# Kernel tuning notes

Hardware: AMD Instinct MI355X
Metric: run time of the kernel (lower is better)

Reference implementation:

```python
import jax, jax.numpy as jnp
import numpy as np

B, S, D, H, L = 8, 1024, 768, 12, 12
HD = D // H          # head dim 64
F = 4 * D            # mlp hidden 3072
N_SEG = 8            # ~images packed per sequence


def layer_norm(x, w, b, eps=1e-5):
    m = jnp.mean(x, axis=-1, keepdims=True)
    v = jnp.mean((x - m) ** 2, axis=-1, keepdims=True)
    return (x - m) / jnp.sqrt(v + eps) * w + b


def setup_inputs() -> dict:
    key = jax.random.key(0)
    ks = jax.random.split(key, 16)
    packed_tokens = jax.random.normal(ks[0], (B, S, D), dtype=jnp.float32)
    # block-diagonal mask from sorted segment ids (True = disallowed, torch bool-mask convention)
    seg = jnp.sort(jax.random.randint(ks[1], (S,), 0, N_SEG))
    attn_mask = seg[:, None] != seg[None, :]
    std = 0.02
    p = {
        'packed_tokens': packed_tokens,
        'attn_mask': attn_mask,
        'ln1_w': jnp.ones((L, D), jnp.float32),
        'ln1_b': jnp.zeros((L, D), jnp.float32),
        'wqkv': jax.random.normal(ks[2], (L, D, 3 * D), jnp.float32) * std,
        'bqkv': jnp.zeros((L, 3 * D), jnp.float32),
        'wo': jax.random.normal(ks[3], (L, D, D), jnp.float32) * std,
        'bo': jnp.zeros((L, D), jnp.float32),
        'ln2_w': jnp.ones((L, D), jnp.float32),
        'ln2_b': jnp.zeros((L, D), jnp.float32),
        'w1': jax.random.normal(ks[4], (L, D, F), jnp.float32) * std,
        'b1': jnp.zeros((L, F), jnp.float32),
        'w2': jax.random.normal(ks[5], (L, F, D), jnp.float32) * std,
        'b2': jnp.zeros((L, D), jnp.float32),
        'norm_w': jnp.ones((D,), jnp.float32),
        'norm_b': jnp.zeros((D,), jnp.float32),
    }
    return p


def attention(x, mask, wqkv, bqkv, wo, bo):
    qkv = x @ wqkv + bqkv                                  # [B,S,3D]
    q, k, v = jnp.split(qkv, 3, axis=-1)
    q = q.reshape(B, S, H, HD)
    k = k.reshape(B, S, H, HD)
    v = v.reshape(B, S, H, HD)
    scores = jnp.einsum('bqhd,bkhd->bhqk', q, k) / jnp.sqrt(jnp.asarray(HD, x.dtype))
    neg = jnp.asarray(jnp.finfo(scores.dtype).min, scores.dtype)
    scores = jnp.where(mask[None, None], neg, scores)
    probs = jax.nn.softmax(scores, axis=-1)
    out = jnp.einsum('bhqk,bkhd->bqhd', probs, v).reshape(B, S, D)
    return out @ wo + bo


def reference(packed_tokens, attn_mask, ln1_w, ln1_b, wqkv, bqkv, wo, bo,
              ln2_w, ln2_b, w1, b1, w2, b2, norm_w, norm_b):
    x = packed_tokens  # dropout = identity in eval
    for l in range(L):
        n = layer_norm(x, ln1_w[l], ln1_b[l])
        x = x + attention(n, attn_mask, wqkv[l], bqkv[l], wo[l], bo[l])
        n = layer_norm(x, ln2_w[l], ln2_b[l])
        h = jax.nn.gelu(n @ w1[l] + b1[l], approximate=False)
        x = x + h @ w2[l] + b2[l]
    return layer_norm(x, norm_w, norm_b)
```

## Files before the change

### kernel.cpp

```cpp
#include <hip/hip_runtime.h>
#include <hip/hip_bf16.h>
#include <math.h>

typedef __hip_bfloat16 bf16_t;
typedef _Float16 h16;
typedef _Float16 f16x8 __attribute__((ext_vector_type(8)));
typedef float f32x4 __attribute__((ext_vector_type(4)));

constexpr int B = 8;
constexpr int S = 1024;
constexpr int D = 768;
constexpr int H = 12;
constexpr int HD = 64;
constexpr int F = 3072;
constexpr int L = 12;
constexpr int T = B * S;


typedef const __attribute__((address_space(1))) void g_void;
typedef __attribute__((address_space(3))) void s_void;
#define GLD16(gp, lp) __builtin_amdgcn_global_load_lds((g_void*)(gp), (s_void*)(lp), 16, 0, 0)

__device__ __forceinline__ float ldf(const void* p, size_t i, int f32) {
    return f32 ? ((const float*)p)[i] : __bfloat162float(((const bf16_t*)p)[i]);
}

__global__ void dtype_sniff_kernel(const uint32_t* __restrict__ w, int* __restrict__ meta) {
    if (threadIdx.x == 0) meta[1] = (w[0] == 0x3F800000u) ? 1 : 0;
}

__global__ __launch_bounds__(256) void mask_sniff_kernel(const uint32_t* __restrict__ mask,
                                                         int* __restrict__ meta) {
    __shared__ int firstw;
    if (threadIdx.x == 0) firstw = 1 << 30;
    __syncthreads();
    int idx = threadIdx.x;
    uint32_t v0 = mask[idx];
    uint32_t v1 = mask[256 + idx];
    uint32_t v2 = mask[512 + idx];
    uint32_t v3 = mask[768 + idx];
    int best = 1 << 30;
    if (v3) best = 768 + idx;
    if (v2) best = 512 + idx;
    if (v1) best = 256 + idx;
    if (v0) best = idx;
    atomicMin(&firstw, best);
    __syncthreads();
    if (threadIdx.x == 0) {
        int fi = firstw;
        meta[0] = (fi < (1 << 30) && mask[fi] == 1u) ? 1 : 0;
    }
}

__global__ __launch_bounds__(256) void rowrange_kernel(const void* __restrict__ mask,
                                                       int* __restrict__ meta) {
    int q = blockIdx.x;
    int f = meta[0];
    int lo = S, hi = -1;
    for (int j = threadIdx.x; j < S; j += 256) {
        int v = f ? ((const int*)mask)[(size_t)q * S + j]
                  : (int)((const unsigned char*)mask)[(size_t)q * S + j];
        if (v == 0) { lo = min(lo, j); hi = max(hi, j); }
    }
    for (int off = 32; off > 0; off >>= 1) {
        lo = min(lo, __shfl_xor(lo, off));
        hi = max(hi, __shfl_xor(hi, off));
    }
    __shared__ int slo[4], shi[4];
    int wv = threadIdx.x >> 6;
    if ((threadIdx.x & 63) == 0) { slo[wv] = lo; shi[wv] = hi; }
    __syncthreads();
    if (threadIdx.x == 0) {
        lo = min(min(slo[0], slo[1]), min(slo[2], slo[3]));
        hi = max(max(shi[0], shi[1]), max(shi[2], shi[3]));
        if (lo > hi) { lo = q; hi = q; }
        meta[16 + q] = lo;
        meta[16 + S + q] = hi;
    }
}

__global__ __launch_bounds__(256) void cast_kernel(const void* __restrict__ in,
                                                   const int* __restrict__ meta,
                                                   float* __restrict__ out, int n) {
    int f32 = meta[1];
    int i = blockIdx.x * 256 + threadIdx.x;
    if (i < n) out[i] = ldf(in, i, f32);
}

template <bool EXTERNAL>
__global__ __launch_bounds__(256) void ln_kernel(const float* __restrict__ x,
                                                 const void* __restrict__ w, size_t wo_,
                                                 const void* __restrict__ b, size_t bo_,
                                                 const int* __restrict__ meta,
                                                 void* __restrict__ out) {
    int f32 = meta[1];
    int t = blockIdx.x;
    int tid = threadIdx.x;
    __shared__ float xs[D];
    __shared__ float red[16];
    const float* xp = x + (size_t)t * D;

    float s = 0.f;
#pragma unroll
    for (int i = 0; i < 3; i++) {
        float v = xp[tid + i * 256];
        xs[tid + i * 256] = v;
        s += v;
    }
    for (int off = 32; off > 0; off >>= 1) s += __shfl_xor(s, off);
    int wv = tid >> 6, lane = tid & 63;
    if (lane == 0) red[wv] = s;
    __syncthreads();
    float mean = (red[0] + red[1] + red[2] + red[3]) * (1.0f / 768.0f);

    float s2 = 0.f;
#pragma unroll
    for (int i = 0; i < 3; i++) {
        float d = xs[tid + i * 256] - mean;
        s2 += d * d;
    }
    for (int off = 32; off > 0; off >>= 1) s2 += __shfl_xor(s2, off);
    if (lane == 0) red[8 + wv] = s2;
    __syncthreads();
    float var = (red[8] + red[9] + red[10] + red[11]) * (1.0f / 768.0f);
    float rstd = rsqrtf(var + 1e-5f);

#pragma unroll
    for (int i = 0; i < 3; i++) {
        int d = tid + i * 256;
        float v = (xs[d] - mean) * rstd * ldf(w, wo_ + d, f32) + ldf(b, bo_ + d, f32);
        size_t idx = (size_t)t * D + d;
        if (EXTERNAL) {
            if (f32) ((float*)out)[idx] = v;
            else ((bf16_t*)out)[idx] = __float2bfloat16(v);
        } else {
            ((h16*)out)[idx] = (h16)v;
        }
    }
}

__global__ __launch_bounds__(256) void wtrans_kernel(const void* __restrict__ W, size_t woff,
                                                     const int* __restrict__ meta,
                                                     h16* __restrict__ wt,
                                                     int K, int N) {
    int f32 = meta[1];
    __shared__ float tile[32][33];
    int n0 = blockIdx.x * 32, k0 = blockIdx.y * 32;
    int tx = threadIdx.x & 31, ty = threadIdx.x >> 5;
#pragma unroll
    for (int i = 0; i < 4; i++) {
        int k = ty + i * 8;
        tile[k][tx] = ldf(W, woff + (size_t)(k0 + k) * N + n0 + tx, f32);
    }
    __syncthreads();
#pragma unroll
    for (int i = 0; i < 4; i++) {
        int nn = ty + i * 8;
        wt[(size_t)(n0 + nn) * K + k0 + tx] = (h16)tile[tx][nn];
    }
}

template <bool GELU, bool ADD>
__global__ __launch_bounds__(256) void mgemm_kernel(const h16* __restrict__ A,
                                                    const h16* __restrict__ Bt,
                                                    const void* __restrict__ bias, size_t boff,
                                                    const int* __restrict__ meta,
                                                    void* __restrict__ C,
                                                    int M, int N, int K) {
    int f32 = meta[1];
    __shared__ h16 Als[128 * 32];
    __shared__ h16 Bls[128 * 32];
    int tid = threadIdx.x;
    int lane = tid & 63;
    int wv = tid >> 6;
    int wy = wv >> 1, wx = wv & 1;
    int m0 = blockIdx.y * 128, n0 = blockIdx.x * 128;

    int row0 = tid >> 2, kc0 = (tid & 3) * 8;
    int row1 = 64 + row0;
    const h16* ag0 = A + (size_t)(m0 + row0) * K + kc0;
    const h16* ag1 = A + (size_t)(m0 + row1) * K + kc0;
    const h16* bg0 = Bt + (size_t)(n0 + row0) * K + kc0;
    const h16* bg1 = Bt + (size_t)(n0 + row1) * K + kc0;
    h16* la0 = Als + (size_t)tid * 8;
    h16* la1 = Als + (size_t)(256 + tid) * 8;
    h16* lb0 = Bls + (size_t)tid * 8;
    h16* lb1 = Bls + (size_t)(256 + tid) * 8;

    const h16* pa = Als + ((wy * 64) + (lane & 15)) * 32 + (lane >> 4) * 8;
    const h16* pb = Bls + ((wx * 64) + (lane & 15)) * 32 + (lane >> 4) * 8;

    f32x4 acc[4][4];
#pragma unroll
    for (int i = 0; i < 4; i++)
#pragma unroll
        for (int j = 0; j < 4; j++) acc[i][j] = (f32x4){0.f, 0.f, 0.f, 0.f};

    for (int k0 = 0; k0 < K; k0 += 32) {
        GLD16(ag0, la0); GLD16(ag1, la1);
        GLD16(bg0, lb0); GLD16(bg1, lb1);
        ag0 += 32; ag1 += 32; bg0 += 32; bg1 += 32;
        __syncthreads();

        f16x8 af[4], bf[4];
#pragma unroll
        for (int i = 0; i < 4; i++) af[i] = *(const f16x8*)(pa + i * 16 * 32);
#pragma unroll
        for (int j = 0; j < 4; j++) bf[j] = *(const f16x8*)(pb + j * 16 * 32);
#pragma unroll
        for (int i = 0; i < 4; i++)
#pragma unroll
            for (int j = 0; j < 4; j++)
                acc[i][j] = __builtin_amdgcn_mfma_f32_16x16x32_f16(af[i], bf[j], acc[i][j], 0, 0, 0);
        __syncthreads();
    }

    int col_base = n0 + wx * 64 + (lane & 15);
    int row_base = m0 + wy * 64 + (lane >> 4) * 4;
#pragma unroll
    for (int j = 0; j < 4; j++) {
        int nn = col_base + j * 16;
        float bv = ldf(bias, boff + nn, f32);
#pragma unroll
        for (int i = 0; i < 4; i++) {
#pragma unroll
            for (int r = 0; r < 4; r++) {
                int mm = row_base + i * 16 + r;
                float v = acc[i][j][r] + bv;
                if (GELU) v = 0.5f * v * (1.0f + erff(v * 0.70710678118654752f));
                size_t idx = (size_t)mm * N + nn;
                if (ADD) ((float*)C)[idx] += v;
                else ((h16*)C)[idx] = (h16)v;
            }
        }
    }
}

template <bool GELU, bool ADD>
__global__ __launch_bounds__(256) void gemm_kernel(const h16* __restrict__ A,
                                                   const void* __restrict__ W, size_t wo_,
                                                   const void* __restrict__ bias, size_t bo_,
                                                   const int* __restrict__ meta,
                                                   void* __restrict__ C,
                                                   int M, int N, int K) {
    int f32 = meta[1];
    __shared__ float As[16][65];
    __shared__ float Bs[16][65];
    int tid = threadIdx.y * 16 + threadIdx.x;
    int m0 = blockIdx.y * 64, n0 = blockIdx.x * 64;
    float c[4][4] = {};

    for (int k0 = 0; k0 < K; k0 += 16) {
#pragma unroll
        for (int i = 0; i < 4; i++) {
            int flat = tid + i * 256;
            int m = flat >> 4, k = flat & 15;
            As[k][m] = (float)A[(size_t)(m0 + m) * K + k0 + k];
        }
#pragma unroll
        for (int i = 0; i < 4; i++) {
            int flat = tid + i * 256;
            int k = flat >> 6, n = flat & 63;
            Bs[k][n] = ldf(W, wo_ + (size_t)(k0 + k) * N + n0 + n, f32);
        }
        __syncthreads();
#pragma unroll
        for (int kk = 0; kk < 16; kk++) {
            float a[4], bb[4];
#pragma unroll
            for (int i = 0; i < 4; i++) a[i] = As[kk][threadIdx.y * 4 + i];
#pragma unroll
            for (int j = 0; j < 4; j++) bb[j] = Bs[kk][threadIdx.x * 4 + j];
#pragma unroll
            for (int i = 0; i < 4; i++)
#pragma unroll
                for (int j = 0; j < 4; j++) c[i][j] += a[i] * bb[j];
        }
        __syncthreads();
    }

#pragma unroll
    for (int i = 0; i < 4; i++) {
        int m = m0 + threadIdx.y * 4 + i;
#pragma unroll
        for (int j = 0; j < 4; j++) {
            int n = n0 + threadIdx.x * 4 + j;
            float v = c[i][j] + ldf(bias, bo_ + n, f32);
            if (GELU) v = 0.5f * v * (1.0f + erff(v * 0.70710678118654752f));
            size_t idx = (size_t)m * N + n;
            if (ADD) ((float*)C)[idx] += v;
            else ((h16*)C)[idx] = (h16)v;
        }
    }
}

__global__ __launch_bounds__(256) void mattn_kernel(const h16* __restrict__ qkv,
                                                    const int* __restrict__ meta,
                                                    h16* __restrict__ ao) {
    const int* rowlo = meta + 16;
    const int* rowhi = meta + 16 + S;
    int bh = blockIdx.y;
    int b = bh / H, h = bh % H;
    int q0 = blockIdx.x * 64;
    int tid = threadIdx.x;
    int lane = tid & 63;
    int w = tid >> 6;
    int qw = q0 + w * 16;

    __shared__ h16 Vt[64 * 64];
    __shared__ h16 Ps[4][16 * 64];

    const size_t rs = 3 * D;
    const h16* base = qkv + (size_t)b * S * rs;

    int rl = rowlo[q0 + lane], rh = rowhi[q0 + lane];
    for (int off = 32; off > 0; off >>= 1) {
        rl = min(rl, __shfl_xor(rl, off));
        rh = max(rh, __shfl_xor(rh, off));
    }
    int c_lo = rl & ~63;
    int c_hi = rh + 1;

    int qrow = qw + (lane >> 4) * 4;
    int mlo[4], mhi[4];
#pragma unroll
    for (int r = 0; r < 4; r++) { mlo[r] = rowlo[qrow + r]; mhi[r] = rowhi[qrow + r]; }

    f16x8 qf[2];
    {
        const h16* qp = base + (size_t)(qw + (lane & 15)) * rs + h * 64 + (lane >> 4) * 8;
        qf[0] = *(const f16x8*)(qp);
        qf[1] = *(const f16x8*)(qp + 32);
    }

    float m_r[4], l_r[4];
    f32x4 o[4];
#pragma unroll
    for (int r = 0; r < 4; r++) { m_r[r] = -1e30f; l_r[r] = 0.f; }
#pragma unroll
    for (int jf = 0; jf < 4; jf++) o[jf] = (f32x4){0.f, 0.f, 0.f, 0.f};

    for (int c0 = c_lo; c0 < c_hi; c0 += 64) {
        {
            int k = tid & 63, d0 = (tid >> 6) * 16;
            const h16* vp = base + (size_t)(c0 + k) * rs + 2 * D + h * 64 + d0;
            f16x8 v0 = *(const f16x8*)vp;
            f16x8 v1 = *(const f16x8*)(vp + 8);
#pragma unroll
            for (int j = 0; j < 8; j++) {
                int d = d0 + j;
                Vt[(d * 64 + k) ^ ((d & 7) << 3)] = v0[j];
                d = d0 + 8 + j;
                Vt[(d * 64 + k) ^ ((d & 7) << 3)] = v1[j];
            }
        }

        f32x4 s[4];
#pragma unroll
        for (int jf = 0; jf < 4; jf++) {
            const h16* kp = base + (size_t)(c0 + jf * 16 + (lane & 15)) * rs + D + h * 64 + (lane >> 4) * 8;
            f16x8 kf0 = *(const f16x8*)kp;
            f16x8 kf1 = *(const f16x8*)(kp + 32);
            s[jf] = (f32x4){0.f, 0.f, 0.f, 0.f};
            s[jf] = __builtin_amdgcn_mfma_f32_16x16x32_f16(qf[0], kf0, s[jf], 0, 0, 0);
            s[jf] = __builtin_amdgcn_mfma_f32_16x16x32_f16(qf[1], kf1, s[jf], 0, 0, 0);
        }

        float pmax[4];
#pragma unroll
        for (int r = 0; r < 4; r++) pmax[r] = -3.0e38f;
#pragma unroll
        for (int jf = 0; jf < 4; jf++) {
            int k = c0 + jf * 16 + (lane & 15);
#pragma unroll
            for (int r = 0; r < 4; r++) {
                float v = (k < mlo[r] || k > mhi[r]) ? -3.0e38f : s[jf][r] * 0.125f;
                s[jf][r] = v;
                pmax[r] = fmaxf(pmax[r], v);
            }
        }
#pragma unroll
        for (int off = 1; off < 16; off <<= 1)
#pragma unroll
            for (int r = 0; r < 4; r++) pmax[r] = fmaxf(pmax[r], __shfl_xor(pmax[r], off));

        float scl[4];
#pragma unroll
        for (int r = 0; r < 4; r++) {
            float mn = fmaxf(m_r[r], pmax[r]);
            scl[r] = __expf(m_r[r] - mn);
            m_r[r] = mn;
            l_r[r] *= scl[r];
        }
#pragma unroll
        for (int jf = 0; jf < 4; jf++) {
#pragma unroll
            for (int r = 0; r < 4; r++) {
                float e = __expf(s[jf][r] - m_r[r]);
                l_r[r] += e;
                int q = (lane >> 4) * 4 + r;
                int k = jf * 16 + (lane & 15);
                Ps[w][(q * 64 + k) ^ ((q & 7) << 3)] = (h16)e;
            }
        }
#pragma unroll
        for (int jf = 0; jf < 4; jf++)
#pragma unroll
            for (int r = 0; r < 4; r++) o[jf][r] *= scl[r];

        __syncthreads();

        f16x8 pa0, pa1;
        {
            int q = lane & 15;
            int e0 = q * 64 + (lane >> 4) * 8;
            int e1 = q * 64 + 32 + (lane >> 4) * 8;
            pa0 = *(const f16x8*)&Ps[w][e0 ^ ((q & 7) << 3)];
            pa1 = *(const f16x8*)&Ps[w][e1 ^ ((q & 7) << 3)];
        }
#pragma unroll
        for (int jf = 0; jf < 4; jf++) {
            int d = jf * 16 + (lane & 15);
            int e0 = d * 64 + (lane >> 4) * 8;
            int e1 = d * 64 + 32 + (lane >> 4) * 8;
            f16x8 vb0 = *(const f16x8*)&Vt[e0 ^ ((d & 7) << 3)];
            f16x8 vb1 = *(const f16x8*)&Vt[e1 ^ ((d & 7) << 3)];
            o[jf] = __builtin_amdgcn_mfma_f32_16x16x32_f16(pa0, vb0, o[jf], 0, 0, 0);
            o[jf] = __builtin_amdgcn_mfma_f32_16x16x32_f16(pa1, vb1, o[jf], 0, 0, 0);
        }
        __syncthreads();
    }

#pragma unroll
    for (int off = 1; off < 16; off <<= 1)
#pragma unroll
        for (int r = 0; r < 4; r++) l_r[r] += __shfl_xor(l_r[r], off);
#pragma unroll
    for (int jf = 0; jf < 4; jf++) {
        int d = jf * 16 + (lane & 15);
#pragma unroll
        for (int r = 0; r < 4; r++) {
            float inv = (l_r[r] > 0.f) ? 1.0f / l_r[r] : 0.f;
            int q = qw + (lane >> 4) * 4 + r;
            ao[(size_t)(b * S + q) * D + h * 64 + d] = (h16)(o[jf][r] * inv);
        }
    }
}

__global__ __launch_bounds__(512) void attn_kernel(const h16* __restrict__ qkv,
                                                   const int* __restrict__ meta,
                                                   h16* __restrict__ ao) {
    const int* rowlo = meta + 16;
    const int* rowhi = meta + 16 + S;
    int bh = blockIdx.x;
    int b = bh / H, h = bh % H;
    int q0 = blockIdx.y * 8;
    int tid = threadIdx.x;
    int qr = tid >> 6;
    int lane = tid & 63;
    int q = q0 + qr;

    __shared__ float qs[8][64];
    __shared__ float sc[8][S];
    __shared__ float kv[64][65];

    const size_t rowstride = 3 * D;
    const h16* qkv_b = qkv + (size_t)b * S * rowstride;

    qs[qr][lane] = (float)qkv_b[(size_t)(q0 + qr) * rowstride + h * 64 + lane];

    int lo = rowlo[q], hi = rowhi[q];
    int blo = S, bhi = -1;
#pragma unroll
    for (int i = 0; i < 8; i++) {
        blo = min(blo, rowlo[q0 + i]);
        bhi = max(bhi, rowhi[q0 + i]);
    }
    int c_lo = (blo / 64) * 64;
    int c_hi = bhi + 1;
    int c_up = c_lo + ((c_hi - c_lo + 63) / 64) * 64;

    for (int c0 = c_lo; c0 < c_hi; c0 += 64) {
        __syncthreads();
#pragma unroll
        for (int i = 0; i < 8; i++) {
            int flat = tid + i * 512;
            int jj = flat >> 6, dd = flat & 63;
            kv[jj][dd] = (float)qkv_b[(size_t)(c0 + jj) * rowstride + D + h * 64 + dd];
        }
        __syncthreads();
        float acc = 0.f;
#pragma unroll
        for (int d = 0; d < 64; d++) acc += qs[qr][d] * kv[lane][d];
        int j = c0 + lane;
        bool msk = (j < lo) || (j > hi);
        sc[qr][j] = msk ? -3.0e38f : acc * 0.125f;
    }
    __syncthreads();

    float m = -3.4e38f;
    for (int j = c_lo + lane; j < c_up; j += 64) m = fmaxf(m, sc[qr][j]);
    for (int off = 32; off > 0; off >>= 1) m = fmaxf(m, __shfl_xor(m, off));
    float sum = 0.f;
    for (int j = c_lo + lane; j < c_up; j += 64) {
        float e = expf(sc[qr][j] - m);
        sc[qr][j] = e;
        sum += e;
    }
    for (int off = 32; off > 0; off >>= 1) sum += __shfl_xor(sum, off);
    float inv = (sum > 0.f) ? 1.0f / sum : 0.f;

    float out = 0.f;
    for (int c0 = c_lo; c0 < c_hi; c0 += 64) {
        __syncthreads();
#pragma unroll
        for (int i = 0; i < 8; i++) {
            int flat = tid + i * 512;
            int jj = flat >> 6, dd = flat & 63;
            kv[jj][dd] = (float)qkv_b[(size_t)(c0 + jj) * rowstride + 2 * D + h * 64 + dd];
        }
        __syncthreads();
#pragma unroll
        for (int jj = 0; jj < 64; jj++) out += sc[qr][c0 + jj] * kv[jj][lane];
    }
    out *= inv;
    ao[((size_t)(b * S + q)) * D + h * 64 + lane] = (h16)out;
}

__global__ __launch_bounds__(256) void sentinel_kernel(uint32_t* __restrict__ out, int nwords) {
    int i = blockIdx.x * 256 + threadIdx.x;
    if (i < nwords) out[i] = 0x3F803F80u;
}

extern "C" void kernel_launch(void* const* d_in, const int* in_sizes, int n_in,
                              void* d_out, int out_size, void* d_ws, size_t ws_size,
                              hipStream_t stream) {
    const void* packed = d_in[0];
    const void* mask   = d_in[1];
    const void* ln1w   = d_in[2];
    const void* ln1b   = d_in[3];
    const void* wqkv   = d_in[4];
    const void* bqkv   = d_in[5];
    const void* wo     = d_in[6];
    const void* bo     = d_in[7];
    const void* ln2w   = d_in[8];
    const void* ln2b   = d_in[9];
    const void* w1     = d_in[10];
    const void* b1     = d_in[11];
    const void* w2     = d_in[12];
    const void* b2     = d_in[13];
    const void* normw  = d_in[14];
    const void* normb  = d_in[15];

    size_t x_b   = (size_t)T * D * 4;
    size_t n_b   = (size_t)T * D * 2;
    size_t big_b = (size_t)T * F * 2;
    size_t need_old = 16384 + x_b + n_b + big_b;
    size_t wt_elems = (size_t)3 * D * D + (size_t)D * D + (size_t)D * F + (size_t)F * D;
    size_t need_new = need_old + wt_elems * 2 ;

    if (ws_size < need_old) {
        int nwords = out_size / 2;
        sentinel_kernel<<<(nwords + 255) / 256, 256, 0, stream>>>((uint32_t*)d_out, nwords);
        return;
    }

    int* meta = (int*)d_ws;
    float* x  = (float*)((char*)d_ws + 16384);
    h16* n    = (h16*)((char*)x + x_b);
    h16* big  = (h16*)((char*)n + n_b);

    dtype_sniff_kernel<<<1, 64, 0, stream>>>((const uint32_t*)ln1w, meta);
    mask_sniff_kernel<<<1, 256, 0, stream>>>((const uint32_t*)mask, meta);
    rowrange_kernel<<<S, 256, 0, stream>>>(mask, meta);
    cast_kernel<<<(T * D + 255) / 256, 256, 0, stream>>>(packed, meta, x, T * D);

    if (ws_size >= need_new) {
        h16* wts = (h16*)((char*)big + big_b);
        h16* qkvT = wts;
        h16* woT  = qkvT + (size_t)3 * D * D;
        h16* w1T  = woT + (size_t)D * D;
        h16* w2T  = w1T + (size_t)D * F;

        for (int l = 0; l < L; l++) {
            wtrans_kernel<<<dim3(3 * D / 32, D / 32), 256, 0, stream>>>(
                wqkv, (size_t)l * D * 3 * D, meta, qkvT, D, 3 * D);
            wtrans_kernel<<<dim3(D / 32, D / 32), 256, 0, stream>>>(
                wo, (size_t)l * D * D, meta, woT, D, D);
            wtrans_kernel<<<dim3(F / 32, D / 32), 256, 0, stream>>>(
                w1, (size_t)l * D * F, meta, w1T, D, F);
            wtrans_kernel<<<dim3(D / 32, F / 32), 256, 0, stream>>>(
                w2, (size_t)l * F * D, meta, w2T, F, D);

            ln_kernel<false><<<T, 256, 0, stream>>>(x, ln1w, (size_t)l * D, ln1b, (size_t)l * D, meta, n);
            mgemm_kernel<false, false><<<dim3(3 * D / 128, T / 128), 256, 0, stream>>>(
                n, qkvT, bqkv, (size_t)l * 3 * D, meta, big, T, 3 * D, D);
            mattn_kernel<<<dim3(S / 64, B * H), 256, 0, stream>>>(big, meta, n);
            mgemm_kernel<false, true><<<dim3(D / 128, T / 128), 256, 0, stream>>>(
                n, woT, bo, (size_t)l * D, meta, x, T, D, D);
            ln_kernel<false><<<T, 256, 0, stream>>>(x, ln2w, (size_t)l * D, ln2b, (size_t)l * D, meta, n);
            mgemm_kernel<true, false><<<dim3(F / 128, T / 128), 256, 0, stream>>>(
                n, w1T, b1, (size_t)l * F, meta, big, T, F, D);
            mgemm_kernel<false, true><<<dim3(D / 128, T / 128), 256, 0, stream>>>(
                big, w2T, b2, (size_t)l * D, meta, x, T, D, F);
        }
    } else {
        dim3 thr(16, 16);
        for (int l = 0; l < L; l++) {
            ln_kernel<false><<<T, 256, 0, stream>>>(x, ln1w, (size_t)l * D, ln1b, (size_t)l * D, meta, n);
            gemm_kernel<false, false><<<dim3(3 * D / 64, T / 64), thr, 0, stream>>>(
                n, wqkv, (size_t)l * D * 3 * D, bqkv, (size_t)l * 3 * D, meta, big, T, 3 * D, D);
            attn_kernel<<<dim3(B * H, S / 8), 512, 0, stream>>>(big, meta, n);
            gemm_kernel<false, true><<<dim3(D / 64, T / 64), thr, 0, stream>>>(
                n, wo, (size_t)l * D * D, bo, (size_t)l * D, meta, x, T, D, D);
            ln_kernel<false><<<T, 256, 0, stream>>>(x, ln2w, (size_t)l * D, ln2b, (size_t)l * D, meta, n);
            gemm_kernel<true, false><<<dim3(F / 64, T / 64), thr, 0, stream>>>(
                n, w1, (size_t)l * D * F, b1, (size_t)l * F, meta, big, T, F, D);
            gemm_kernel<false, true><<<dim3(D / 64, T / 64), thr, 0, stream>>>(
                big, w2, (size_t)l * F * D, b2, (size_t)l * D, meta, x, T, D, F);
        }
    }
    ln_kernel<true><<<T, 256, 0, stream>>>(x, normw, 0, normb, 0, meta, d_out);
}
```

Measured before the change: 4.473 ms.

## Double-buffer MFMA GEMM LDS, swizzle layout, and split-K residual GEMMs with atomics

Adds a two-stage LDS double buffer so global-to-LDS loads of the next K tile overlap MFMA work on the current one, dropping one barrier per iteration. Applies an XOR swizzle to the LDS K offsets to cut bank conflicts on the fragment reads. Splits K for the output projection (2-way) and the second MLP GEMM (4-way) across blockIdx.z, accumulating into the fp32 residual with atomicAdd, so these 6x64-tile GEMMs get more blocks. Atomics add contention and make the summation order nondeterministic.

```diff
diff --git a/kernel.cpp b/kernel.cpp
--- a/kernel.cpp
+++ b/kernel.cpp
@@ -166,29 +166,29 @@
                                                     const void* __restrict__ bias, size_t boff,
                                                     const int* __restrict__ meta,
                                                     void* __restrict__ C,
-                                                    int M, int N, int K) {
+                                                    int M, int N, int K, int Kc) {
     int f32 = meta[1];
-    __shared__ h16 Als[128 * 32];
-    __shared__ h16 Bls[128 * 32];
+    __shared__ h16 Als[2][128 * 32];
+    __shared__ h16 Bls[2][128 * 32];
     int tid = threadIdx.x;
     int lane = tid & 63;
     int wv = tid >> 6;
     int wy = wv >> 1, wx = wv & 1;
     int m0 = blockIdx.y * 128, n0 = blockIdx.x * 128;
-
-    int row0 = tid >> 2, kc0 = (tid & 3) * 8;
+    int kz = blockIdx.z * Kc;
+
+    int row0 = tid >> 2;
     int row1 = 64 + row0;
-    const h16* ag0 = A + (size_t)(m0 + row0) * K + kc0;
-    const h16* ag1 = A + (size_t)(m0 + row1) * K + kc0;
-    const h16* bg0 = Bt + (size_t)(n0 + row0) * K + kc0;
-    const h16* bg1 = Bt + (size_t)(n0 + row1) * K + kc0;
-    h16* la0 = Als + (size_t)tid * 8;
-    h16* la1 = Als + (size_t)(256 + tid) * 8;
-    h16* lb0 = Bls + (size_t)tid * 8;
-    h16* lb1 = Bls + (size_t)(256 + tid) * 8;
-
-    const h16* pa = Als + ((wy * 64) + (lane & 15)) * 32 + (lane >> 4) * 8;
-    const h16* pb = Bls + ((wx * 64) + (lane & 15)) * 32 + (lane >> 4) * 8;
+    int kbs = (((tid & 3) * 16) ^ ((row0 & 3) << 4)) >> 1;
+    const h16* ag0 = A + (size_t)(m0 + row0) * K + kz + kbs;
+    const h16* ag1 = A + (size_t)(m0 + row1) * K + kz + kbs;
+    const h16* bg0 = Bt + (size_t)(n0 + row0) * K + kz + kbs;
+    const h16* bg1 = Bt + (size_t)(n0 + row1) * K + kz + kbs;
+
+    int arow = (lane & 15);
+    int akb = ((((lane >> 4) * 16) ^ ((arow & 3) << 4)) >> 1);
+    int aoff = (wy * 64 + arow) * 32 + akb;
+    int boff2 = (wx * 64 + arow) * 32 + akb;
 
     f32x4 acc[4][4];
 #pragma unroll
@@ -196,12 +196,25 @@
 #pragma unroll
         for (int j = 0; j < 4; j++) acc[i][j] = (f32x4){0.f, 0.f, 0.f, 0.f};
 
-    for (int k0 = 0; k0 < K; k0 += 32) {
-        GLD16(ag0, la0); GLD16(ag1, la1);
-        GLD16(bg0, lb0); GLD16(bg1, lb1);
-        ag0 += 32; ag1 += 32; bg0 += 32; bg1 += 32;
-        __syncthreads();
-
+    int nst = Kc >> 5;
+    GLD16(ag0, &Als[0][(size_t)tid * 8]);
+    GLD16(ag1, &Als[0][(size_t)(256 + tid) * 8]);
+    GLD16(bg0, &Bls[0][(size_t)tid * 8]);
+    GLD16(bg1, &Bls[0][(size_t)(256 + tid) * 8]);
+    __syncthreads();
+
+    int cur = 0;
+    for (int t = 0; t < nst; ++t) {
+        if (t + 1 < nst) {
+            int nb = cur ^ 1;
+            int off = (t + 1) * 32;
+            GLD16(ag0 + off, &Als[nb][(size_t)tid * 8]);
+            GLD16(ag1 + off, &Als[nb][(size_t)(256 + tid) * 8]);
+            GLD16(bg0 + off, &Bls[nb][(size_t)tid * 8]);
+            GLD16(bg1 + off, &Bls[nb][(size_t)(256 + tid) * 8]);
+        }
+        const h16* pa = cur ? &Als[1][aoff] : &Als[0][aoff];
+        const h16* pb = cur ? &Bls[1][boff2] : &Bls[0][boff2];
         f16x8 af[4], bf[4];
 #pragma unroll
         for (int i = 0; i < 4; i++) af[i] = *(const f16x8*)(pa + i * 16 * 32);
@@ -213,6 +226,7 @@
             for (int j = 0; j < 4; j++)
                 acc[i][j] = __builtin_amdgcn_mfma_f32_16x16x32_f16(af[i], bf[j], acc[i][j], 0, 0, 0);
         __syncthreads();
+        cur ^= 1;
     }
 
     int col_base = n0 + wx * 64 + (lane & 15);
@@ -220,7 +234,7 @@
 #pragma unroll
     for (int j = 0; j < 4; j++) {
         int nn = col_base + j * 16;
-        float bv = ldf(bias, boff + nn, f32);
+        float bv = (blockIdx.z == 0) ? ldf(bias, boff + nn, f32) : 0.f;
 #pragma unroll
         for (int i = 0; i < 4; i++) {
 #pragma unroll
@@ -229,7 +243,7 @@
                 float v = acc[i][j][r] + bv;
                 if (GELU) v = 0.5f * v * (1.0f + erff(v * 0.70710678118654752f));
                 size_t idx = (size_t)mm * N + nn;
-                if (ADD) ((float*)C)[idx] += v;
+                if (ADD) atomicAdd(&((float*)C)[idx], v);
                 else ((h16*)C)[idx] = (h16)v;
             }
         }
@@ -593,16 +607,16 @@
                 w2, (size_t)l * F * D, meta, w2T, F, D);
 
             ln_kernel<false><<<T, 256, 0, stream>>>(x, ln1w, (size_t)l * D, ln1b, (size_t)l * D, meta, n);
-            mgemm_kernel<false, false><<<dim3(3 * D / 128, T / 128), 256, 0, stream>>>(
-                n, qkvT, bqkv, (size_t)l * 3 * D, meta, big, T, 3 * D, D);
+            mgemm_kernel<false, false><<<dim3(3 * D / 128, T / 128, 1), 256, 0, stream>>>(
+                n, qkvT, bqkv, (size_t)l * 3 * D, meta, big, T, 3 * D, D, D);
             mattn_kernel<<<dim3(S / 64, B * H), 256, 0, stream>>>(big, meta, n);
-            mgemm_kernel<false, true><<<dim3(D / 128, T / 128), 256, 0, stream>>>(
-                n, woT, bo, (size_t)l * D, meta, x, T, D, D);
+            mgemm_kernel<false, true><<<dim3(D / 128, T / 128, 2), 256, 0, stream>>>(
+                n, woT, bo, (size_t)l * D, meta, x, T, D, D, D / 2);
             ln_kernel<false><<<T, 256, 0, stream>>>(x, ln2w, (size_t)l * D, ln2b, (size_t)l * D, meta, n);
-            mgemm_kernel<true, false><<<dim3(F / 128, T / 128), 256, 0, stream>>>(
-                n, w1T, b1, (size_t)l * F, meta, big, T, F, D);
-            mgemm_kernel<false, true><<<dim3(D / 128, T / 128), 256, 0, stream>>>(
-                big, w2T, b2, (size_t)l * D, meta, x, T, D, F);
+            mgemm_kernel<true, false><<<dim3(F / 128, T / 128, 1), 256, 0, stream>>>(
+                n, w1T, b1, (size_t)l * F, meta, big, T, F, D, D);
+            mgemm_kernel<false, true><<<dim3(D / 128, T / 128, 4), 256, 0, stream>>>(
+                big, w2T, b2, (size_t)l * D, meta, x, T, D, F, F / 4);
         }
     } else {
         dim3 thr(16, 16);
```

Result: slower. 4.848 ms (+8.4%).
